# Kernel optimization log

Measured on AMD Instinct MI355X. Metric: run time of the kernel, lower is better.

Reference implementation:

```python
import jax, jax.numpy as jnp
import numpy as np

SIGMA = 1.0
SQRT2 = float(np.sqrt(2.0))


def setup_inputs() -> dict:
    key = jax.random.key(0)
    k1, k2 = jax.random.split(key)
    B, L = 128, 1024
    preds = jax.random.normal(k1, (B, L), dtype=jnp.float32)
    # integer relevance grades 0..4, stored as float as in the torch module
    target = jax.random.randint(k2, (B, L), 0, 5).astype(jnp.float32)
    return {"preds": preds, "target": target}


def reference(preds, target):
    B, L = preds.shape
    # pairwise diff [B, L, L]: diff[b,i,j] = preds[b,i] - preds[b,j]
    diff = preds[:, :, None] - preds[:, None, :]
    # Normal(0, sigma*sqrt(2)).cdf(diff) == ndtr(diff / (sigma*sqrt(2)))
    p = jax.scipy.special.ndtr(diff / (SIGMA * SQRT2))
    # zero the diagonal (i == j) before summing
    eye = jnp.eye(L, dtype=bool)
    p = jnp.where(eye[None, :, :], 0.0, p)
    expected_ranks = 1.0 + p.sum(axis=2)  # [B, L]

    gains = 2.0 ** target - 1.0
    discounts = jnp.log2(expected_ranks + 1.0)
    dcg = (gains / discounts).sum(axis=1)  # [B]

    ideal_target = jnp.sort(target, axis=1)[:, ::-1]  # descending
    ideal_gains = 2.0 ** ideal_target - 1.0
    ideal_discounts = jnp.log2(jnp.arange(1, L + 1, dtype=jnp.float32) + 1.0)
    idcg = (ideal_gains / ideal_discounts).sum(axis=1)  # [B]

    ndcg = dcg / (idcg + 1e-10)
    return -ndcg.mean()
```

## Files before the change

### kernel.cpp

```cpp
#include <hip/hip_runtime.h>
#include <hip/hip_fp16.h>

#define B 128
#define L 1024

#if __has_builtin(__builtin_amdgcn_exp2f)
#define EXP2(x) __builtin_amdgcn_exp2f(x)
#else
#define EXP2(x) __expf((x) * 0.6931471805599453f)
#endif

typedef unsigned int uint4v __attribute__((ext_vector_type(4)));

#define WS_ACC  2048
#define WS_GCTR 2049

#define K1f -1.6279072f
#define K2f -0.9299637f
#define K3f -0.1074808f

__device__ __forceinline__ void term2(unsigned int du, __half2 pi2,
                                      __half2 k1, __half2 k2, __half2 k3,
                                      __half2 one2, __half2& acc) {
    __half2 pj = __builtin_bit_cast(__half2, du);
    __half2 d  = __hsub2(pi2, pj);
    unsigned int dbits = __builtin_bit_cast(unsigned int, d);
    __half2 a  = __builtin_bit_cast(__half2, dbits & 0x7fff7fffu);
    __half2 t  = __hfma2(k3, a, k2);
    __half2 u  = __hfma2(t,  a, k1);
    __half2 w  = __hmul2(a, u);
    __half2 e  = __halves2half2(hexp2(__low2half(w)),
                                hexp2(__high2half(w)));
    __half2 r  = __hsub2(one2, e);
    unsigned int rb = __builtin_bit_cast(unsigned int, r) | (dbits & 0x80008000u);
    acc = __hadd2(acc, __builtin_bit_cast(__half2, rb));
}

__global__ __launch_bounds__(256, 8) void pair_kernel(const float* __restrict__ preds,
                                                      const float* __restrict__ target,
                                                      float* __restrict__ ws) {
    __shared__ __align__(16) __half sph[L];
    __shared__ float red[256];

    const int blk  = blockIdx.x;
    const int b    = blk >> 3;
    const int iseg = blk & 7;
    const int tid  = threadIdx.x;
    const int il   = tid & 127;
    const int jh   = tid >> 7;

    if (blk == 0 && tid == 0) {
        ws[WS_ACC] = 0.0f;
        ((int*)ws)[WS_GCTR] = 0;
    }

    const float* prow = preds + b * L;

    float4 v4 = reinterpret_cast<const float4*>(prow)[tid];
    __half2 h01 = __floats2half2_rn(0.5f * v4.x, 0.5f * v4.y);
    __half2 h23 = __floats2half2_rn(0.5f * v4.z, 0.5f * v4.w);
    reinterpret_cast<__half2*>(sph)[tid * 2 + 0] = h01;
    reinterpret_cast<__half2*>(sph)[tid * 2 + 1] = h23;

    const int i = iseg * 128 + il;
    const float tgt = (tid < 128) ? target[b * L + i] : 0.0f;

    __syncthreads();

    const __half2 pi2  = __half2half2(sph[i]);
    const __half2 k1   = __floats2half2_rn(K1f, K1f);
    const __half2 k2   = __floats2half2_rn(K2f, K2f);
    const __half2 k3   = __floats2half2_rn(K3f, K3f);
    const __half2 one2 = __floats2half2_rn(1.0f, 1.0f);
    const __half2 z2   = __floats2half2_rn(0.0f, 0.0f);

    const uint4v* basep = reinterpret_cast<const uint4v*>(sph + jh * 512);

    float E = 0.0f;
    for (int wdw = 0; wdw < 8; ++wdw) {
        __half2 A0 = z2, A1 = z2, A2 = z2, A3 = z2;
        #pragma unroll
        for (int m = 0; m < 8; ++m) {
            uint4v q = basep[wdw * 8 + m];
            term2(q.x, pi2, k1, k2, k3, one2, A0);
            term2(q.y, pi2, k1, k2, k3, one2, A1);
            term2(q.z, pi2, k1, k2, k3, one2, A2);
            term2(q.w, pi2, k1, k2, k3, one2, A3);
        }
        float2 f0 = __half22float2(A0);
        float2 f1 = __half22float2(A1);
        float2 f2 = __half22float2(A2);
        float2 f3 = __half22float2(A3);
        E += ((f0.x + f0.y) + (f1.x + f1.y)) + ((f2.x + f2.y) + (f3.x + f3.y));
    }

    red[tid] = E;
    __syncthreads();

    if (tid < 128) {
        float Es = red[tid] + red[tid + 128];
        float er1 = 513.5f + 0.5f * Es;
        float g = EXP2(tgt) - 1.0f;
        float contrib = g * __builtin_amdgcn_rcpf(__log2f(er1));
        #pragma unroll
        for (int off = 32; off > 0; off >>= 1)
            contrib += __shfl_down(contrib, off);
        if ((tid & 63) == 0)
            ws[blk * 2 + (tid >> 6)] = contrib;
    }
}

__global__ __launch_bounds__(256) void finish_kernel(const float* __restrict__ target,
                                                     float* __restrict__ ws,
                                                     float* __restrict__ out) {
    __shared__ unsigned long long cred[256];
    __shared__ float2 fred[256];

    const int b   = blockIdx.x;
    const int tid = threadIdx.x;
    const float* trow = target + b * L;

    unsigned long long cnt = 0ull;
    #pragma unroll
    for (int k = 0; k < 4; ++k) {
        float t = trow[tid + k * 256];
        cnt += ((unsigned long long)(t > 3.5f) << 48)
             + ((unsigned long long)(t > 2.5f) << 32)
             + ((unsigned long long)(t > 1.5f) << 16)
             + ((unsigned long long)(t > 0.5f));
    }
    cred[tid] = cnt;
    __syncthreads();
    #pragma unroll
    for (int s = 128; s > 0; s >>= 1) {
        if (tid < (unsigned)s) cred[tid] += cred[tid + s];
        __syncthreads();
    }
    unsigned long long tot = cred[0];
    const int n4 = (int)(tot >> 48) & 0xFFFF;
    const int n3 = (int)(tot >> 32) & 0xFFFF;
    const int n2 = (int)(tot >> 16) & 0xFFFF;
    const int n1 = (int)(tot)       & 0xFFFF;

    float idcg_p = 0.0f;
    #pragma unroll
    for (int k = 0; k < 4; ++k) {
        int pos = tid + 1 + k * 256;
        float gain = (pos <= n4) ? 15.0f : (pos <= n3) ? 7.0f :
                     (pos <= n2) ? 3.0f  : (pos <= n1) ? 1.0f : 0.0f;
        idcg_p += gain * __builtin_amdgcn_rcpf(__log2f((float)pos + 1.0f));
    }
    float dcg_p = (tid < 16) ? ws[b * 16 + tid] : 0.0f;
    fred[tid] = make_float2(idcg_p, dcg_p);
    __syncthreads();
    #pragma unroll
    for (int s = 128; s > 0; s >>= 1) {
        if (tid < (unsigned)s) {
            float2 x = fred[tid], y = fred[tid + s];
            fred[tid] = make_float2(x.x + y.x, x.y + y.y);
        }
        __syncthreads();
    }

    if (tid == 0) {
        float ndcg = fred[0].y / (fred[0].x + 1e-10f);
        atomicAdd(&ws[WS_ACC], ndcg);
        __threadfence();
        int old = atomicAdd((int*)ws + WS_GCTR, 1);
        if (old == B - 1) {
            float acc = atomicAdd(&ws[WS_ACC], 0.0f);
            out[0] = -acc * (1.0f / (float)B);
        }
    }
}

extern "C" void kernel_launch(void* const* d_in, const int* in_sizes, int n_in,
                              void* d_out, int out_size, void* d_ws, size_t ws_size,
                              hipStream_t stream) {
    const float* preds  = (const float*)d_in[0];
    const float* target = (const float*)d_in[1];
    float* out = (float*)d_out;
    float* ws  = (float*)d_ws;

    pair_kernel<<<B * 8, 256, 0, stream>>>(preds, target, ws);
    finish_kernel<<<B, 256, 0, stream>>>(target, ws, out);
}
```

Before: 88.57 us.

## Split pair kernel into 16 row segments with four j-quarters per block

Each block now handles 64 rows instead of 128, with four thread groups each covering a quarter of the j range, and the grid doubles to 2048 blocks. The inner loop loads two 16-byte vectors per step into eight half2 accumulators, which gives more independent work per thread. The intent is more blocks to fill the GPU and more instruction-level parallelism. In exchange, every block reloads and converts the full preds row, and the half2 partial sums still cover the same number of terms before being converted to float.

```diff
diff --git a/kernel.cpp b/kernel.cpp
--- a/kernel.cpp
+++ b/kernel.cpp
@@ -43,11 +43,11 @@
     __shared__ float red[256];
 
     const int blk  = blockIdx.x;
-    const int b    = blk >> 3;
-    const int iseg = blk & 7;
+    const int b    = blk >> 4;
+    const int iseg = blk & 15;
     const int tid  = threadIdx.x;
-    const int il   = tid & 127;
-    const int jh   = tid >> 7;
+    const int il   = tid & 63;
+    const int jq   = tid >> 6;
 
     if (blk == 0 && tid == 0) {
         ws[WS_ACC] = 0.0f;
@@ -62,8 +62,8 @@
     reinterpret_cast<__half2*>(sph)[tid * 2 + 0] = h01;
     reinterpret_cast<__half2*>(sph)[tid * 2 + 1] = h23;
 
-    const int i = iseg * 128 + il;
-    const float tgt = (tid < 128) ? target[b * L + i] : 0.0f;
+    const int i = iseg * 64 + il;
+    const float tgt = (tid < 64) ? target[b * L + iseg * 64 + tid] : 0.0f;
 
     __syncthreads();
 
@@ -74,39 +74,46 @@
     const __half2 one2 = __floats2half2_rn(1.0f, 1.0f);
     const __half2 z2   = __floats2half2_rn(0.0f, 0.0f);
 
-    const uint4v* basep = reinterpret_cast<const uint4v*>(sph + jh * 512);
+    const uint4v* basep = reinterpret_cast<const uint4v*>(sph + jq * 256);
 
     float E = 0.0f;
-    for (int wdw = 0; wdw < 8; ++wdw) {
-        __half2 A0 = z2, A1 = z2, A2 = z2, A3 = z2;
+    for (int wdw = 0; wdw < 2; ++wdw) {
+        __half2 A0 = z2, A1 = z2, A2 = z2, A3 = z2,
+                A4 = z2, A5 = z2, A6 = z2, A7 = z2;
         #pragma unroll
         for (int m = 0; m < 8; ++m) {
-            uint4v q = basep[wdw * 8 + m];
-            term2(q.x, pi2, k1, k2, k3, one2, A0);
-            term2(q.y, pi2, k1, k2, k3, one2, A1);
-            term2(q.z, pi2, k1, k2, k3, one2, A2);
-            term2(q.w, pi2, k1, k2, k3, one2, A3);
+            uint4v q0 = basep[wdw * 16 + m * 2 + 0];
+            uint4v q1 = basep[wdw * 16 + m * 2 + 1];
+            term2(q0.x, pi2, k1, k2, k3, one2, A0);
+            term2(q0.y, pi2, k1, k2, k3, one2, A1);
+            term2(q0.z, pi2, k1, k2, k3, one2, A2);
+            term2(q0.w, pi2, k1, k2, k3, one2, A3);
+            term2(q1.x, pi2, k1, k2, k3, one2, A4);
+            term2(q1.y, pi2, k1, k2, k3, one2, A5);
+            term2(q1.z, pi2, k1, k2, k3, one2, A6);
+            term2(q1.w, pi2, k1, k2, k3, one2, A7);
         }
-        float2 f0 = __half22float2(A0);
-        float2 f1 = __half22float2(A1);
-        float2 f2 = __half22float2(A2);
-        float2 f3 = __half22float2(A3);
-        E += ((f0.x + f0.y) + (f1.x + f1.y)) + ((f2.x + f2.y) + (f3.x + f3.y));
+        float2 f0 = __half22float2(A0), f1 = __half22float2(A1);
+        float2 f2 = __half22float2(A2), f3 = __half22float2(A3);
+        float2 f4 = __half22float2(A4), f5 = __half22float2(A5);
+        float2 f6 = __half22float2(A6), f7 = __half22float2(A7);
+        E += (((f0.x + f0.y) + (f1.x + f1.y)) + ((f2.x + f2.y) + (f3.x + f3.y)))
+           + (((f4.x + f4.y) + (f5.x + f5.y)) + ((f6.x + f6.y) + (f7.x + f7.y)));
     }
 
     red[tid] = E;
     __syncthreads();
 
-    if (tid < 128) {
-        float Es = red[tid] + red[tid + 128];
+    if (tid < 64) {
+        float Es = (red[tid] + red[tid + 64]) + (red[tid + 128] + red[tid + 192]);
         float er1 = 513.5f + 0.5f * Es;
         float g = EXP2(tgt) - 1.0f;
         float contrib = g * __builtin_amdgcn_rcpf(__log2f(er1));
         #pragma unroll
         for (int off = 32; off > 0; off >>= 1)
             contrib += __shfl_down(contrib, off);
-        if ((tid & 63) == 0)
-            ws[blk * 2 + (tid >> 6)] = contrib;
+        if (tid == 0)
+            ws[blk] = contrib;
     }
 }
 
@@ -182,6 +189,6 @@
     float* out = (float*)d_out;
     float* ws  = (float*)d_ws;
 
-    pair_kernel<<<B * 8, 256, 0, stream>>>(preds, target, ws);
+    pair_kernel<<<B * 16, 256, 0, stream>>>(preds, target, ws);
     finish_kernel<<<B, 256, 0, stream>>>(target, ws, out);
 }
```

Result: no change. 87.44 us (-1.3%).
